# Kernel optimization log

Measured on AMD Instinct MI355X. Metric: run time of the kernel, lower is better.

Reference implementation:

```python
import jax, jax.numpy as jnp
import numpy as np
import math

DIM = 1024
HEADS = 16
SEQ_LEN = 2048
NUM_PV = 32
HEAD_DIM = DIM // HEADS
EPS = 1e-5


def setup_inputs() -> dict:
    key = jax.random.key(0)
    k1, k2 = jax.random.split(key)
    B = 4
    L = SEQ_LEN + NUM_PV
    x = jax.random.normal(k1, (B, L, DIM), dtype=jnp.float32)
    paramvecs = jax.random.normal(k2, (1, NUM_PV, DIM), dtype=jnp.float32)
    return {"x": x, "paramvecs": paramvecs}


def _layernorm_noaffine(x):
    mu = jnp.mean(x, axis=-1, keepdims=True)
    var = jnp.mean(jnp.square(x - mu), axis=-1, keepdims=True)
    return (x - mu) * jax.lax.rsqrt(var + EPS)


def reference(x, paramvecs):
    B, L, D = x.shape  # L = SEQ_LEN + NUM_PV
    # add learned param vectors onto the trailing num_paramvec positions
    x = x.at[:, SEQ_LEN:, :].add(paramvecs)
    residual = x
    xn = _layernorm_noaffine(x)
    # shared Q = K = V = xn, split into heads: [B, H, L, Dh]
    h = xn.reshape(B, L, HEADS, HEAD_DIM).transpose(0, 2, 1, 3)
    scores = jnp.einsum('bhqd,bhkd->bhqk', h, h) / math.sqrt(HEAD_DIM)
    weights = jax.nn.softmax(scores, axis=-1)
    context = jnp.einsum('bhqk,bhkd->bhqd', weights, h)
    context = context.transpose(0, 2, 1, 3).reshape(B, L, D)
    return context + residual
```

## Files before the change

### kernel.cpp

```cpp
#include <hip/hip_runtime.h>
#include <hip/hip_fp16.h>

#define DIMF 1024
#define NHEADS 16
#define SEQ 2048
#define NPV 32
#define HD 64
#define LTOT 2080
#define LP 2112
#define NB 4
#define BHN 64
#define NQT 33
#define QB 128
#define NQB 17
#define NKV32 66

typedef _Float16 f16x8 __attribute__((ext_vector_type(8)));
typedef float f32x16 __attribute__((ext_vector_type(16)));
typedef unsigned short u16x8 __attribute__((ext_vector_type(8)));
typedef int v2i __attribute__((ext_vector_type(2)));

#if __has_builtin(__builtin_amdgcn_exp2f)
#define EXP2(x) __builtin_amdgcn_exp2f(x)
#else
#define EXP2(x) exp2f(x)
#endif

#define CEXP 0.1803368801111f
#define KSH  11.5415603271f

__global__ __launch_bounds__(256) void prep_kernel(const float* __restrict__ x,
                                                   const float* __restrict__ pv,
                                                   float* __restrict__ out,
                                                   unsigned short* __restrict__ xnh) {
  int row = blockIdx.x;
  int b = row / LP, l = row - b * LP;
  int t = threadIdx.x;
  int h = t >> 4;
  int dd = (t & 15) << 2;
  unsigned short* dst = xnh + ((size_t)(b * NHEADS + h) * LP + l) * HD + dd;
  if (l >= LTOT) {
    *reinterpret_cast<ushort4*>(dst) = make_ushort4(0, 0, 0, 0);
    return;
  }
  const float* xr = x + ((size_t)b * LTOT + l) * DIMF + t * 4;
  float4 v = *reinterpret_cast<const float4*>(xr);
  if (l >= SEQ) {
    float4 p = *reinterpret_cast<const float4*>(pv + (size_t)(l - SEQ) * DIMF + t * 4);
    v.x += p.x; v.y += p.y; v.z += p.z; v.w += p.w;
  }
  *reinterpret_cast<float4*>(out + ((size_t)b * LTOT + l) * DIMF + t * 4) = v;

  float s1 = v.x + v.y + v.z + v.w;
  float s2 = v.x * v.x + v.y * v.y + v.z * v.z + v.w * v.w;
#pragma unroll
  for (int o = 1; o < 64; o <<= 1) { s1 += __shfl_xor(s1, o); s2 += __shfl_xor(s2, o); }
  __shared__ float red[8];
  int wv = t >> 6;
  if ((t & 63) == 0) { red[wv] = s1; red[4 + wv] = s2; }
  __syncthreads();
  s1 = red[0] + red[1] + red[2] + red[3];
  s2 = red[4] + red[5] + red[6] + red[7];
  float mu = s1 * (1.0f / DIMF);
  float var = s2 * (1.0f / DIMF) - mu * mu;
  float rs = rsqrtf(var + 1e-5f);
  ushort4 o4;
  o4.x = __half_as_ushort(__float2half((v.x - mu) * rs));
  o4.y = __half_as_ushort(__float2half((v.y - mu) * rs));
  o4.z = __half_as_ushort(__float2half((v.z - mu) * rs));
  o4.w = __half_as_ushort(__float2half((v.w - mu) * rs));
  *reinterpret_cast<ushort4*>(dst) = o4;
}

__global__ __launch_bounds__(256) void transpose_kernel(const unsigned short* __restrict__ xnh,
                                                        unsigned short* __restrict__ xnt) {
  __shared__ unsigned short tile[64][72];
  int blk = blockIdx.x;
  int bh = blk / NQT, lt = blk - bh * NQT;
  int t = threadIdx.x;
  int rr = t >> 3;
  int c8 = (t & 7) << 3;
#pragma unroll
  for (int p = 0; p < 2; p++) {
    int ll = rr + p * 32;
    float4 v = *reinterpret_cast<const float4*>(xnh + ((size_t)bh * LP + lt * 64 + ll) * HD + c8);
    int cs = c8 ^ (((ll >> 3) & 7) << 3);
    *reinterpret_cast<float4*>(&tile[ll][cs]) = v;
  }
  __syncthreads();
  int l8 = (t & 7) << 3;
#pragma unroll
  for (int p = 0; p < 2; p++) {
    int d = rr + p * 32;
    u16x8 o;
#pragma unroll
    for (int j = 0; j < 8; j++) {
      o[j] = tile[l8 + j][d ^ ((t & 7) << 3)];
    }
    *reinterpret_cast<u16x8*>(xnt + ((size_t)bh * HD + d) * LP + lt * 64 + l8) = o;
  }
}

static __device__ __forceinline__ f32x16 mfma32(f16x8 a, f16x8 b, f32x16 c) {
  return __builtin_amdgcn_mfma_f32_32x32x16_f16(a, b, c, 0, 0, 0);
}

static __device__ __forceinline__ unsigned cvtpk(float a, float b) {
  auto h = __builtin_amdgcn_cvt_pkrtz(a, b);
  return __builtin_bit_cast(unsigned, h);
}

static __device__ __forceinline__ void pack2(const f32x16& P, f16x8& f0, f16x8& f1) {
  unsigned a0 = cvtpk(P[0], P[1]),  b0 = cvtpk(P[4], P[5]);
  unsigned a1 = cvtpk(P[2], P[3]),  b1 = cvtpk(P[6], P[7]);
  v2i s0 = __builtin_amdgcn_permlane32_swap(a0, b0, false, false);
  v2i s1 = __builtin_amdgcn_permlane32_swap(a1, b1, false, false);
  unsigned a2 = cvtpk(P[8], P[9]),   b2 = cvtpk(P[12], P[13]);
  unsigned a3 = cvtpk(P[10], P[11]), b3 = cvtpk(P[14], P[15]);
  v2i s2 = __builtin_amdgcn_permlane32_swap(a2, b2, false, false);
  v2i s3 = __builtin_amdgcn_permlane32_swap(a3, b3, false, false);
  union { unsigned u[4]; f16x8 v; } u0, u1;
  u0.u[0] = (unsigned)s0.x; u0.u[1] = (unsigned)s1.x; u0.u[2] = (unsigned)s0.y; u0.u[3] = (unsigned)s1.y;
  u1.u[0] = (unsigned)s2.x; u1.u[1] = (unsigned)s3.x; u1.u[2] = (unsigned)s2.y; u1.u[3] = (unsigned)s3.y;
  f0 = u0.v; f1 = u1.v;
}

#define GLDS(src, dst) \
  __builtin_amdgcn_global_load_lds( \
      (const __attribute__((address_space(1))) unsigned int*)(src), \
      (__attribute__((address_space(3))) unsigned int*)(dst), 16, 0, 0)

__device__ __forceinline__ void kv_step16(const unsigned short* kbuf, const unsigned short* vbuf,
                                          const f16x8 (&qf)[4], f32x16& accA, f32x16& accB,
                                          float& rowsum, int l31, int hi, int sw) {
  const unsigned short* k0 = kbuf + (size_t)l31 * 64;
  f32x16 st = {};
  __builtin_amdgcn_s_setprio(1);
#pragma unroll
  for (int ds = 0; ds < 4; ds++) {
    int cl = ds * 2 + hi;
    f16x8 ka = *reinterpret_cast<const f16x8*>(k0 + ((cl ^ sw) << 3));
    st = mfma32(ka, qf[ds], st);
  }
  __builtin_amdgcn_s_setprio(0);
#pragma unroll
  for (int r = 0; r < 16; r++) {
    st[r] = EXP2(st[r] * CEXP - KSH);
    rowsum += st[r];
  }
  f16x8 pa[2];
  pack2(st, pa[0], pa[1]);
  const unsigned short* v0 = vbuf + (size_t)l31 * 64;
  __builtin_amdgcn_s_setprio(1);
#pragma unroll
  for (int ks = 0; ks < 2; ks++) {
    int clA = ks * 2 + hi;
    f16x8 bvA = *reinterpret_cast<const f16x8*>(v0 + ((clA ^ sw) << 3));
    accA = mfma32(pa[ks], bvA, accA);
    int clB = 4 + ks * 2 + hi;
    f16x8 bvB = *reinterpret_cast<const f16x8*>(v0 + ((clB ^ sw) << 3));
    accB = mfma32(pa[ks], bvB, accB);
  }
  __builtin_amdgcn_s_setprio(0);
}

__global__ __launch_bounds__(256, 4) void attn_kernel(const unsigned short* __restrict__ xnh,
                                                      const unsigned short* __restrict__ xnt,
                                                      float* __restrict__ out) {
  __shared__ unsigned short kt0[32 * 64], kt1[32 * 64];
  __shared__ unsigned short vt0[32 * 64], vt1[32 * 64];
  __shared__ float wred[4][32];
  int bid = blockIdx.x;
  const int nwg = BHN * NQB;
  const int cpx = nwg >> 3;
  int wg = (bid & 7) * cpx + (bid >> 3);
  int bh = wg / NQB, qt = wg - bh * NQB;
  int b = bh >> 4, h = bh & 15;
  int tid = threadIdx.x;
  int wid = tid >> 6;
  int lane = tid & 63;
  int l31 = lane & 31, hi = lane >> 5;
  int sw = l31 & 7;
  int q0w = qt * QB + wid * 32;
  const unsigned short* Kb = xnh + (size_t)bh * (LP * HD);
  const unsigned short* Vb = xnt + (size_t)bh * (HD * LP);

  f16x8 qf[4];
#pragma unroll
  for (int ds = 0; ds < 4; ds++)
    qf[ds] = *reinterpret_cast<const f16x8*>(Kb + (size_t)(q0w + l31) * HD + ds * 16 + hi * 8);

  f32x16 accA = {};
  f32x16 accB = {};
  float rowsum = 0.f;

  int r = tid >> 3, cp = tid & 7;
  int cl = cp ^ (r & 7);
  const unsigned short* pK = Kb + (size_t)r * HD + cl * 8;
  const unsigned short* pV = Vb + (size_t)(r + 32 * (cl >> 2)) * LP + (cl & 3) * 8;
  unsigned short* dK0 = kt0 + (size_t)wid * 512;
  unsigned short* dK1 = kt1 + (size_t)wid * 512;
  unsigned short* dV0 = vt0 + (size_t)wid * 512;
  unsigned short* dV1 = vt1 + (size_t)wid * 512;

#define STAGE0() do { GLDS(pK, dK0); GLDS(pV, dV0); pK += 32 * HD; pV += 32; } while (0)
#define STAGE1() do { GLDS(pK, dK1); GLDS(pV, dV1); pK += 32 * HD; pV += 32; } while (0)

  STAGE0();
  __syncthreads();

  for (int it = 0; it < 32; ++it) {
    STAGE1();
    kv_step16(kt0, vt0, qf, accA, accB, rowsum, l31, hi, sw);
    __syncthreads();
    STAGE0();
    kv_step16(kt1, vt1, qf, accA, accB, rowsum, l31, hi, sw);
    __syncthreads();
  }
  STAGE1();
  kv_step16(kt0, vt0, qf, accA, accB, rowsum, l31, hi, sw);
  __syncthreads();
  kv_step16(kt1, vt1, qf, accA, accB, rowsum, l31, hi, sw);

  float full = rowsum + __shfl_xor(rowsum, 32);
  full -= 32.0f * exp2f(-KSH);
  float inv = 1.0f / full;
  if (lane < 32) wred[wid][l31] = inv;
  float* obase = out + (size_t)b * LTOT * DIMF + h * HD + l31;
  if (q0w < LTOT) {
#pragma unroll
    for (int q2 = 0; q2 < 4; q2++) {
      float4 iv = *reinterpret_cast<const float4*>(&wred[wid][q2 * 8 + hi * 4]);
#pragma unroll
      for (int j = 0; j < 4; j++) {
        int qg = q0w + q2 * 8 + hi * 4 + j;
        float* p = obase + (size_t)qg * DIMF;
        float ivj = (j == 0) ? iv.x : (j == 1) ? iv.y : (j == 2) ? iv.z : iv.w;
        p[0]  += accA[q2 * 4 + j] * ivj;
        p[32] += accB[q2 * 4 + j] * ivj;
      }
    }
  }
#undef STAGE0
#undef STAGE1
}

extern "C" void kernel_launch(void* const* d_in, const int* in_sizes, int n_in,
                              void* d_out, int out_size, void* d_ws, size_t ws_size,
                              hipStream_t stream) {
  const float* x  = (const float*)d_in[0];
  const float* pv = (const float*)d_in[1];
  float* out = (float*)d_out;
  unsigned short* xnh = (unsigned short*)d_ws;
  unsigned short* xnt = xnh + (size_t)BHN * LP * HD;
  prep_kernel<<<NB * LP, 256, 0, stream>>>(x, pv, out, xnh);
  transpose_kernel<<<BHN * NQT, 256, 0, stream>>>(xnh, xnt);
  attn_kernel<<<BHN * NQB, 256, 0, stream>>>(xnh, xnt, out);
}
```

Before: 128.1 us.

## Deepen KV staging to four-buffer ring with explicit vmcnt waits

```diff
diff --git a/kernel.cpp b/kernel.cpp
--- a/kernel.cpp
+++ b/kernel.cpp
@@ -167,8 +167,8 @@
 __global__ __launch_bounds__(256, 4) void attn_kernel(const unsigned short* __restrict__ xnh,
                                                       const unsigned short* __restrict__ xnt,
                                                       float* __restrict__ out) {
-  __shared__ unsigned short kt0[32 * 64], kt1[32 * 64];
-  __shared__ unsigned short vt0[32 * 64], vt1[32 * 64];
+  __shared__ unsigned short kts[4][32 * 64];
+  __shared__ unsigned short vts[4][32 * 64];
   __shared__ float wred[4][32];
   int bid = blockIdx.x;
   const int nwg = BHN * NQB;
@@ -198,29 +198,33 @@
   int cl = cp ^ (r & 7);
   const unsigned short* pK = Kb + (size_t)r * HD + cl * 8;
   const unsigned short* pV = Vb + (size_t)(r + 32 * (cl >> 2)) * LP + (cl & 3) * 8;
-  unsigned short* dK0 = kt0 + (size_t)wid * 512;
-  unsigned short* dK1 = kt1 + (size_t)wid * 512;
-  unsigned short* dV0 = vt0 + (size_t)wid * 512;
-  unsigned short* dV1 = vt1 + (size_t)wid * 512;
-
-#define STAGE0() do { GLDS(pK, dK0); GLDS(pV, dV0); pK += 32 * HD; pV += 32; } while (0)
-#define STAGE1() do { GLDS(pK, dK1); GLDS(pV, dV1); pK += 32 * HD; pV += 32; } while (0)
-
-  STAGE0();
-  __syncthreads();
-
-  for (int it = 0; it < 32; ++it) {
-    STAGE1();
-    kv_step16(kt0, vt0, qf, accA, accB, rowsum, l31, hi, sw);
-    __syncthreads();
-    STAGE0();
-    kv_step16(kt1, vt1, qf, accA, accB, rowsum, l31, hi, sw);
-    __syncthreads();
-  }
-  STAGE1();
-  kv_step16(kt0, vt0, qf, accA, accB, rowsum, l31, hi, sw);
-  __syncthreads();
-  kv_step16(kt1, vt1, qf, accA, accB, rowsum, l31, hi, sw);
+  int widoff = wid * 512;
+
+#define STAGE(bi) do { GLDS(pK, kts[bi] + widoff); GLDS(pV, vts[bi] + widoff); \
+                       pK += 32 * HD; pV += 32; } while (0)
+
+#define BODY(t, bi) do { \
+    asm volatile("s_waitcnt vmcnt(4)" ::: "memory"); \
+    __builtin_amdgcn_s_barrier(); \
+    if ((t) + 3 < NKV32) STAGE(((t) + 3) & 3); \
+    kv_step16(kts[bi], vts[bi], qf, accA, accB, rowsum, l31, hi, sw); \
+  } while (0)
+
+  STAGE(0); STAGE(1); STAGE(2);
+
+  for (int it = 0; it < 16; ++it) {
+    int t0 = it * 4;
+    BODY(t0 + 0, 0);
+    BODY(t0 + 1, 1);
+    BODY(t0 + 2, 2);
+    BODY(t0 + 3, 3);
+  }
+  asm volatile("s_waitcnt vmcnt(2)" ::: "memory");
+  __builtin_amdgcn_s_barrier();
+  kv_step16(kts[0], vts[0], qf, accA, accB, rowsum, l31, hi, sw);
+  asm volatile("s_waitcnt vmcnt(0)" ::: "memory");
+  __builtin_amdgcn_s_barrier();
+  kv_step16(kts[1], vts[1], qf, accA, accB, rowsum, l31, hi, sw);
 
   float full = rowsum + __shfl_xor(rowsum, 32);
   full -= 32.0f * exp2f(-KSH);
@@ -241,8 +245,8 @@
       }
     }
   }
-#undef STAGE0
-#undef STAGE1
+#undef STAGE
+#undef BODY
 }
 
 extern "C" void kernel_launch(void* const* d_in, const int* in_sizes, int n_in,
```

Result: slower. 146.6 us (+14.4%).

## Fold softmax scale into Q and compute row sums with MFMA

Applied to the files above, without the earlier changes.

```diff
diff --git a/kernel.cpp b/kernel.cpp
--- a/kernel.cpp
+++ b/kernel.cpp
@@ -13,7 +13,7 @@
 #define NQT 33
 #define QB 128
 #define NQB 17
-#define NKV32 66
+#define NKV 65
 
 typedef _Float16 f16x8 __attribute__((ext_vector_type(8)));
 typedef float f32x16 __attribute__((ext_vector_type(16)));
@@ -132,9 +132,13 @@
 
 __device__ __forceinline__ void kv_step16(const unsigned short* kbuf, const unsigned short* vbuf,
                                           const f16x8 (&qf)[4], f32x16& accA, f32x16& accB,
-                                          float& rowsum, int l31, int hi, int sw) {
+                                          f32x16& accS, int l31, int hi, int sw) {
+  const _Float16 one = (_Float16)1.0f;
+  const f16x8 onesv = {one, one, one, one, one, one, one, one};
   const unsigned short* k0 = kbuf + (size_t)l31 * 64;
-  f32x16 st = {};
+  f32x16 st;
+#pragma unroll
+  for (int r = 0; r < 16; r++) st[r] = -KSH;
   __builtin_amdgcn_s_setprio(1);
 #pragma unroll
   for (int ds = 0; ds < 4; ds++) {
@@ -144,14 +148,13 @@
   }
   __builtin_amdgcn_s_setprio(0);
 #pragma unroll
-  for (int r = 0; r < 16; r++) {
-    st[r] = EXP2(st[r] * CEXP - KSH);
-    rowsum += st[r];
-  }
+  for (int r = 0; r < 16; r++) st[r] = EXP2(st[r]);
   f16x8 pa[2];
   pack2(st, pa[0], pa[1]);
   const unsigned short* v0 = vbuf + (size_t)l31 * 64;
   __builtin_amdgcn_s_setprio(1);
+  accS = mfma32(pa[0], onesv, accS);
+  accS = mfma32(pa[1], onesv, accS);
 #pragma unroll
   for (int ks = 0; ks < 2; ks++) {
     int clA = ks * 2 + hi;
@@ -169,7 +172,6 @@
                                                       float* __restrict__ out) {
   __shared__ unsigned short kt0[32 * 64], kt1[32 * 64];
   __shared__ unsigned short vt0[32 * 64], vt1[32 * 64];
-  __shared__ float wred[4][32];
   int bid = blockIdx.x;
   const int nwg = BHN * NQB;
   const int cpx = nwg >> 3;
@@ -186,13 +188,17 @@
   const unsigned short* Vb = xnt + (size_t)bh * (HD * LP);
 
   f16x8 qf[4];
-#pragma unroll
-  for (int ds = 0; ds < 4; ds++)
+  const _Float16 ce = (_Float16)CEXP;
+  const f16x8 cev = {ce, ce, ce, ce, ce, ce, ce, ce};
+#pragma unroll
+  for (int ds = 0; ds < 4; ds++) {
     qf[ds] = *reinterpret_cast<const f16x8*>(Kb + (size_t)(q0w + l31) * HD + ds * 16 + hi * 8);
+    qf[ds] = qf[ds] * cev;
+  }
 
   f32x16 accA = {};
   f32x16 accB = {};
-  float rowsum = 0.f;
+  f32x16 accS = {};
 
   int r = tid >> 3, cp = tid & 7;
   int cl = cp ^ (r & 7);
@@ -211,33 +217,26 @@
 
   for (int it = 0; it < 32; ++it) {
     STAGE1();
-    kv_step16(kt0, vt0, qf, accA, accB, rowsum, l31, hi, sw);
+    kv_step16(kt0, vt0, qf, accA, accB, accS, l31, hi, sw);
     __syncthreads();
     STAGE0();
-    kv_step16(kt1, vt1, qf, accA, accB, rowsum, l31, hi, sw);
+    kv_step16(kt1, vt1, qf, accA, accB, accS, l31, hi, sw);
     __syncthreads();
   }
-  STAGE1();
-  kv_step16(kt0, vt0, qf, accA, accB, rowsum, l31, hi, sw);
-  __syncthreads();
-  kv_step16(kt1, vt1, qf, accA, accB, rowsum, l31, hi, sw);
-
-  float full = rowsum + __shfl_xor(rowsum, 32);
-  full -= 32.0f * exp2f(-KSH);
-  float inv = 1.0f / full;
-  if (lane < 32) wred[wid][l31] = inv;
+  kv_step16(kt0, vt0, qf, accA, accB, accS, l31, hi, sw);
+
   float* obase = out + (size_t)b * LTOT * DIMF + h * HD + l31;
   if (q0w < LTOT) {
 #pragma unroll
     for (int q2 = 0; q2 < 4; q2++) {
-      float4 iv = *reinterpret_cast<const float4*>(&wred[wid][q2 * 8 + hi * 4]);
 #pragma unroll
       for (int j = 0; j < 4; j++) {
+        int rr = q2 * 4 + j;
         int qg = q0w + q2 * 8 + hi * 4 + j;
+        float inv = 1.0f / accS[rr];
         float* p = obase + (size_t)qg * DIMF;
-        float ivj = (j == 0) ? iv.x : (j == 1) ? iv.y : (j == 2) ? iv.z : iv.w;
-        p[0]  += accA[q2 * 4 + j] * ivj;
-        p[32] += accB[q2 * 4 + j] * ivj;
+        p[0]  += accA[rr] * inv;
+        p[32] += accB[rr] * inv;
       }
     }
   }
```

After: 185.1 us. 1.44x slower.
